# Kernel optimization log

Hardware: AMD Instinct MI355X
Metric: run time of the kernel (lower is better)

The kernel has to match this reference:

```python
import jax, jax.numpy as jnp
import numpy as np
from jax.ops import segment_sum

IN_DIM, HID_DIM, OUT_DIM = 128, 128, 64
N_NODES, N_EDGES = 50000, 800000


def gcn_conv(x, src, dst, W, b, n_nodes):
    # Symmetric GCN normalization (no self loops): deg at targets from unit weights
    deg = segment_sum(jnp.ones(src.shape[0], dtype=x.dtype), dst, num_segments=n_nodes)
    dinv = jnp.where(deg > 0, jax.lax.rsqrt(jnp.maximum(deg, 1.0)), 0.0)
    norm = dinv[src] * dinv[dst]                      # [E]
    h = x @ W                                         # [N, out] small GEMM first (PyG order)
    msg = h[src] * norm[:, None]                      # gather + scale: [E, out]
    out = segment_sum(msg, dst, num_segments=n_nodes) # scatter-add to targets
    return out + b


def setup_inputs() -> dict:
    key = jax.random.key(0)
    k1, k2, k3, k4, k5 = jax.random.split(key, 5)
    x = jax.random.normal(k1, (N_NODES, IN_DIM), dtype=jnp.float32)
    edge_index = jax.random.randint(k2, (2, N_EDGES), 0, N_NODES, dtype=jnp.int64)
    s1 = 1.0 / np.sqrt(IN_DIM)
    s2 = 1.0 / np.sqrt(HID_DIM)
    W1 = jax.random.uniform(k3, (IN_DIM, HID_DIM), jnp.float32, -s1, s1)
    b1 = jnp.zeros((HID_DIM,), jnp.float32)
    W2 = jax.random.uniform(k4, (HID_DIM, OUT_DIM), jnp.float32, -s2, s2)
    b2 = jnp.zeros((OUT_DIM,), jnp.float32)
    return {"x": x, "edge_index": edge_index, "W1": W1, "b1": b1, "W2": W2, "b2": b2}


def reference(x, edge_index, W1, b1, W2, b2):
    n_nodes = x.shape[0]
    src, dst = edge_index[0], edge_index[1]
    h = gcn_conv(x, src, dst, W1, b1, n_nodes)
    h = jax.nn.relu(h)
    # Dropout is identity in eval mode (reference is deterministic)
    out = gcn_conv(h, src, dst, W2, b2, n_nodes)
    return out
```

## Files before the change

### kernel.cpp

```cpp
#include <hip/hip_runtime.h>

#define N_NODES 50000
#define N_EDGES 800000
#define IN_DIM  128
#define HID_DIM 128
#define OUT_DIM 64

#define NPAD 50176
#define CAP  64
#define GEMM1B ((N_NODES + 63) / 64)
#define FILLB (N_EDGES / 256)
#define W2PREPB 8

typedef __attribute__((ext_vector_type(8))) short bf16x8;
typedef __attribute__((ext_vector_type(4))) float f32x4;
typedef __attribute__((ext_vector_type(2))) float f32x2;

__device__ __forceinline__ unsigned short f2bf(float f) {
    unsigned u = __float_as_uint(f);
    u += 0x7fffu + ((u >> 16) & 1u);
    return (unsigned short)(u >> 16);
}
__device__ __forceinline__ float bflo(unsigned u) { return __uint_as_float(u << 16); }
__device__ __forceinline__ float bfhi(unsigned u) { return __uint_as_float(u & 0xffff0000u); }

#define ACC8(u)  do { \
    acc[0] += bflo(u.x); acc[1] += bfhi(u.x); \
    acc[2] += bflo(u.y); acc[3] += bfhi(u.y); \
    acc[4] += bflo(u.z); acc[5] += bfhi(u.z); \
    acc[6] += bflo(u.w); acc[7] += bfhi(u.w); } while (0)

__device__ __forceinline__ unsigned char f2fp8(float f) {
    return (unsigned char)(__builtin_amdgcn_cvt_pk_fp8_f32(f, f, 0, false) & 0xff);
}

#define ACCF16(u)  do { \
    f32x2 p0 = __builtin_amdgcn_cvt_pk_f32_fp8((int)u.x, false); \
    f32x2 p1 = __builtin_amdgcn_cvt_pk_f32_fp8((int)u.x, true);  \
    f32x2 p2 = __builtin_amdgcn_cvt_pk_f32_fp8((int)u.y, false); \
    f32x2 p3 = __builtin_amdgcn_cvt_pk_f32_fp8((int)u.y, true);  \
    f32x2 p4 = __builtin_amdgcn_cvt_pk_f32_fp8((int)u.z, false); \
    f32x2 p5 = __builtin_amdgcn_cvt_pk_f32_fp8((int)u.z, true);  \
    f32x2 p6 = __builtin_amdgcn_cvt_pk_f32_fp8((int)u.w, false); \
    f32x2 p7 = __builtin_amdgcn_cvt_pk_f32_fp8((int)u.w, true);  \
    acc[0]  += p0[0]; acc[1]  += p0[1]; acc[2]  += p1[0]; acc[3]  += p1[1]; \
    acc[4]  += p2[0]; acc[5]  += p2[1]; acc[6]  += p3[0]; acc[7]  += p3[1]; \
    acc[8]  += p4[0]; acc[9]  += p4[1]; acc[10] += p5[0]; acc[11] += p5[1]; \
    acc[12] += p6[0]; acc[13] += p6[1]; acc[14] += p7[0]; acc[15] += p7[1]; } while (0)

__device__ __forceinline__ float deg2dinv(int deg) {
    return (deg > 0) ? rsqrtf((float)deg) : 0.0f;
}

#define W1T_STRIDE 136


__global__ __launch_bounds__(256) void prep_fill_kernel(const int* __restrict__ src,
                                                        const int* __restrict__ dst,
                                                        int* __restrict__ cnt,
                                                        unsigned short* __restrict__ csr_src,
                                                        const float* __restrict__ W2,
                                                        unsigned short* __restrict__ w2t) {
    int bid = blockIdx.x;
    int tid = threadIdx.x;
    if (bid < W2PREPB) {
        int idx = bid * 256 + tid;
        int c = idx >> 5, k4 = (idx & 31) * 4;
        ushort4 o;
        o.x = f2bf(W2[(k4 + 0) * 64 + c]);
        o.y = f2bf(W2[(k4 + 1) * 64 + c]);
        o.z = f2bf(W2[(k4 + 2) * 64 + c]);
        o.w = f2bf(W2[(k4 + 3) * 64 + c]);
        *(ushort4*)(w2t + c * 128 + k4) = o;
    } else {
        int e = (bid - W2PREPB) * 256 + tid;
        int s = src[e], d = dst[e];
        int slot = atomicAdd(&cnt[d], 1);
        if (slot < CAP) csr_src[(d << 6) + slot] = (unsigned short)s;
    }
}


__global__ __launch_bounds__(256) void gemm1_kernel(const float* __restrict__ x,
                                                    const float* __restrict__ W1,
                                                    const int* __restrict__ cnt,
                                                    unsigned char* __restrict__ h1f8) {
    __shared__ unsigned short w1t[128 * W1T_STRIDE];

    int tid = threadIdx.x;
#pragma unroll
    for (int i = 0; i < 64; ++i) {
        int idx = i * 256 + tid;
        int k = idx >> 7, c = idx & 127;
        w1t[c * W1T_STRIDE + k] = f2bf(W1[idx]);
    }
    __syncthreads();

    int wave = tid >> 6;
    int lane = tid & 63;
    int n = lane & 15, quad = lane >> 4;
    int row0 = blockIdx.x * 64 + wave * 16;

    int arow = row0 + n;
    if (arow >= N_NODES) arow = N_NODES - 1;
    const float* aptr = x + (size_t)arow * 128 + quad * 8;
    const unsigned short* bbase = w1t + (size_t)n * W1T_STRIDE + quad * 8;

    f32x4 acc[8];
#pragma unroll
    for (int t = 0; t < 8; ++t) acc[t] = (f32x4){0.f, 0.f, 0.f, 0.f};

#pragma unroll
    for (int w4 = 0; w4 < 4; ++w4) {
        float4 f0 = *(const float4*)(aptr + w4 * 32);
        float4 f1 = *(const float4*)(aptr + w4 * 32 + 4);
        bf16x8 af;
        af[0] = (short)f2bf(f0.x); af[1] = (short)f2bf(f0.y);
        af[2] = (short)f2bf(f0.z); af[3] = (short)f2bf(f0.w);
        af[4] = (short)f2bf(f1.x); af[5] = (short)f2bf(f1.y);
        af[6] = (short)f2bf(f1.z); af[7] = (short)f2bf(f1.w);
#pragma unroll
        for (int t = 0; t < 8; ++t) {
            bf16x8 bf = *(const bf16x8*)(bbase + (size_t)t * 16 * W1T_STRIDE + w4 * 32);
            acc[t] = __builtin_amdgcn_mfma_f32_16x16x32_bf16(af, bf, acc[t], 0, 0, 0);
        }
    }

#pragma unroll
    for (int r = 0; r < 4; ++r) {
        int row = row0 + quad * 4 + r;
        if (row < N_NODES) {
            float dn = deg2dinv(cnt[row]);
            unsigned char* o = h1f8 + (size_t)row * 128 + n;
#pragma unroll
            for (int t = 0; t < 8; ++t) o[t * 16] = f2fp8(acc[t][r] * dn);
        }
    }
}


#define A1T_STRIDE 136

__global__ __launch_bounds__(1024) void agg1_gemm2_fused(const unsigned short* __restrict__ csr_src,
                                                         const int* __restrict__ cnt,
                                                         const float* __restrict__ b1,
                                                         const unsigned char* __restrict__ h1f8,
                                                         const unsigned short* __restrict__ w2t,
                                                         unsigned short* __restrict__ h2b) {
    __shared__ unsigned short a1t[16 * A1T_STRIDE];

    int node0 = blockIdx.x * 16;
    int wave = threadIdx.x >> 6;
    int lane = threadIdx.x & 63;
    int grp = lane >> 3;
    int q   = lane & 7;
    int node = node0 + wave;
    int start = node << 6;
    int m = cnt[node];
    float dn = deg2dinv(m);
    if (m > CAP) m = CAP;

    float acc[16] = {};
    int j = grp;
    for (; j + 8 < m; j += 16) {
        int s0 = csr_src[start + j];
        int s1 = csr_src[start + j + 8];
        uint4 u0 = ((const uint4*)(h1f8 + (size_t)s0 * 128))[q];
        uint4 u1 = ((const uint4*)(h1f8 + (size_t)s1 * 128))[q];
        ACCF16(u0); ACCF16(u1);
    }
    if (j < m) {
        int s0 = csr_src[start + j];
        uint4 u0 = ((const uint4*)(h1f8 + (size_t)s0 * 128))[q];
        ACCF16(u0);
    }

#pragma unroll
    for (int d = 8; d <= 32; d <<= 1) {
#pragma unroll
        for (int c = 0; c < 16; ++c) acc[c] += __shfl_xor(acc[c], d, 64);
    }

    if (grp == 0) {
        int c0 = q * 16;
        float4 bA = *(const float4*)(b1 + c0);
        float4 bB = *(const float4*)(b1 + c0 + 4);
        float4 bC = *(const float4*)(b1 + c0 + 8);
        float4 bD = *(const float4*)(b1 + c0 + 12);
        ushort4 oA, oB, oC, oD;
        oA.x = f2bf(fmaxf(acc[0]  * dn + bA.x, 0.f));
        oA.y = f2bf(fmaxf(acc[1]  * dn + bA.y, 0.f));
        oA.z = f2bf(fmaxf(acc[2]  * dn + bA.z, 0.f));
        oA.w = f2bf(fmaxf(acc[3]  * dn + bA.w, 0.f));
        oB.x = f2bf(fmaxf(acc[4]  * dn + bB.x, 0.f));
        oB.y = f2bf(fmaxf(acc[5]  * dn + bB.y, 0.f));
        oB.z = f2bf(fmaxf(acc[6]  * dn + bB.z, 0.f));
        oB.w = f2bf(fmaxf(acc[7]  * dn + bB.w, 0.f));
        oC.x = f2bf(fmaxf(acc[8]  * dn + bC.x, 0.f));
        oC.y = f2bf(fmaxf(acc[9]  * dn + bC.y, 0.f));
        oC.z = f2bf(fmaxf(acc[10] * dn + bC.z, 0.f));
        oC.w = f2bf(fmaxf(acc[11] * dn + bC.w, 0.f));
        oD.x = f2bf(fmaxf(acc[12] * dn + bD.x, 0.f));
        oD.y = f2bf(fmaxf(acc[13] * dn + bD.y, 0.f));
        oD.z = f2bf(fmaxf(acc[14] * dn + bD.z, 0.f));
        oD.w = f2bf(fmaxf(acc[15] * dn + bD.w, 0.f));
        ushort4* o = (ushort4*)(a1t + wave * A1T_STRIDE + c0);
        o[0] = oA; o[1] = oB; o[2] = oC; o[3] = oD;
    }
    __syncthreads();

    if (wave < 4) {
        int n = lane & 15, quad = lane >> 4;
        const unsigned short* bbase = w2t + (size_t)(wave * 16 + n) * 128 + quad * 8;
        const unsigned short* abase = a1t + (size_t)n * A1T_STRIDE + quad * 8;

        f32x4 c2 = (f32x4){0.f, 0.f, 0.f, 0.f};
#pragma unroll
        for (int w4 = 0; w4 < 4; ++w4) {
            bf16x8 af = *(const bf16x8*)(abase + w4 * 32);
            bf16x8 bf = *(const bf16x8*)(bbase + w4 * 32);
            c2 = __builtin_amdgcn_mfma_f32_16x16x32_bf16(af, bf, c2, 0, 0, 0);
        }

#pragma unroll
        for (int r = 0; r < 4; ++r) {
            int row = node0 + quad * 4 + r;
            float dr = deg2dinv(cnt[row]);
            h2b[(size_t)row * 64 + wave * 16 + n] = f2bf(c2[r] * dr);
        }
    }
}


__global__ __launch_bounds__(256) void agg2_kernel(const unsigned short* __restrict__ csr_src,
                                                   const int* __restrict__ cnt,
                                                   const float* __restrict__ b2,
                                                   const unsigned short* __restrict__ h2b,
                                                   float* __restrict__ out) {
    int node = blockIdx.x * 4 + (threadIdx.x >> 6);
    if (node >= N_NODES) return;
    int lane = threadIdx.x & 63;
    int grp = lane >> 3;
    int q   = lane & 7;
    int start = node << 6;
    int m = cnt[node];
    float dn = deg2dinv(m);
    if (m > CAP) m = CAP;

    float acc[8] = {};

    int j = grp;
    for (; j + 8 < m; j += 16) {
        int s0 = csr_src[start + j];
        int s1 = csr_src[start + j + 8];
        uint4 u0 = ((const uint4*)(h2b + (size_t)s0 * 64))[q];
        uint4 u1 = ((const uint4*)(h2b + (size_t)s1 * 64))[q];
        ACC8(u0); ACC8(u1);
    }
    if (j < m) {
        int s0 = csr_src[start + j];
        uint4 u0 = ((const uint4*)(h2b + (size_t)s0 * 64))[q];
        ACC8(u0);
    }

#pragma unroll
    for (int d = 8; d <= 32; d <<= 1) {
#pragma unroll
        for (int c = 0; c < 8; ++c) acc[c] += __shfl_xor(acc[c], d, 64);
    }

    if (lane < 8) {
        float4 bA = ((const float4*)b2)[2 * q];
        float4 bB = ((const float4*)b2)[2 * q + 1];
        float4 rA, rB;
        rA.x = acc[0] * dn + bA.x;
        rA.y = acc[1] * dn + bA.y;
        rA.z = acc[2] * dn + bA.z;
        rA.w = acc[3] * dn + bA.w;
        rB.x = acc[4] * dn + bB.x;
        rB.y = acc[5] * dn + bB.y;
        rB.z = acc[6] * dn + bB.z;
        rB.w = acc[7] * dn + bB.w;
        float4* o = (float4*)(out + (size_t)node * 64);
        o[2 * q] = rA;
        o[2 * q + 1] = rB;
    }
}


extern "C" void kernel_launch(void* const* d_in, const int* in_sizes, int n_in,
                              void* d_out, int out_size, void* d_ws, size_t ws_size,
                              hipStream_t stream) {
    const float* x  = (const float*)d_in[0];
    const int*   ei = (const int*)d_in[1];
    const float* W1 = (const float*)d_in[2];
    const float* b1 = (const float*)d_in[3];
    const float* W2 = (const float*)d_in[4];
    const float* b2 = (const float*)d_in[5];
    float* out = (float*)d_out;

    const int* src = ei;
    const int* dst = ei + N_EDGES;

    char* ws = (char*)d_ws;
    int*   cnt       = (int*)ws;
    unsigned short* csr_src = (unsigned short*)(cnt + NPAD);
    unsigned char* h1f8 = (unsigned char*)(csr_src + (size_t)N_NODES * CAP);
    unsigned short* h2b = (unsigned short*)(h1f8 + (size_t)N_NODES * HID_DIM);
    unsigned short* w2t = h2b + (size_t)N_NODES * OUT_DIM;

    (void)hipMemsetAsync(cnt, 0, NPAD * sizeof(int), stream);

    prep_fill_kernel<<<W2PREPB + FILLB, 256, 0, stream>>>(src, dst, cnt, csr_src,
                                                          W2, w2t);

    gemm1_kernel<<<GEMM1B, 256, 0, stream>>>(x, W1, cnt, h1f8);

    agg1_gemm2_fused<<<N_NODES / 16, 1024, 0, stream>>>(csr_src, cnt, b1, h1f8, w2t, h2b);

    agg2_kernel<<<(N_NODES + 3) / 4, 256, 0, stream>>>(csr_src, cnt, b2, h2b, out);
}
```

Baseline: 199.3 us.

## Remap agg1 to 8 lanes per node, dropping cross-lane shuffle reductions

The fused layer-1 aggregation plus GEMM2 kernel now gives each node an 8-lane group instead of a full 64-lane wave, so 32 nodes share a 256-thread block. Each group walks all of its node's edges serially, loading four source indices at once as a ushort4. This removes the three-step shuffle-xor reduction across 16 accumulators and the idle lanes on low-degree nodes. All four waves now run two 16-row MFMA tiles for GEMM2 instead of leaving waves idle. In exchange each lane carries a longer dependent gather chain with less memory-level parallelism per node, and bounds checks are added for the last partial block.

```diff
diff --git a/kernel.cpp b/kernel.cpp
--- a/kernel.cpp
+++ b/kernel.cpp
@@ -11,6 +11,7 @@
 #define GEMM1B ((N_NODES + 63) / 64)
 #define FILLB (N_EDGES / 256)
 #define W2PREPB 8
+#define AGG1B ((N_NODES + 31) / 32)
 
 typedef __attribute__((ext_vector_type(8))) short bf16x8;
 typedef __attribute__((ext_vector_type(4))) float f32x4;
@@ -141,47 +142,44 @@
 
 #define A1T_STRIDE 136
 
-__global__ __launch_bounds__(1024) void agg1_gemm2_fused(const unsigned short* __restrict__ csr_src,
-                                                         const int* __restrict__ cnt,
-                                                         const float* __restrict__ b1,
-                                                         const unsigned char* __restrict__ h1f8,
-                                                         const unsigned short* __restrict__ w2t,
-                                                         unsigned short* __restrict__ h2b) {
-    __shared__ unsigned short a1t[16 * A1T_STRIDE];
-
-    int node0 = blockIdx.x * 16;
-    int wave = threadIdx.x >> 6;
-    int lane = threadIdx.x & 63;
-    int grp = lane >> 3;
-    int q   = lane & 7;
-    int node = node0 + wave;
+__global__ __launch_bounds__(256) void agg1_gemm2_fused(const unsigned short* __restrict__ csr_src,
+                                                        const int* __restrict__ cnt,
+                                                        const float* __restrict__ b1,
+                                                        const unsigned char* __restrict__ h1f8,
+                                                        const unsigned short* __restrict__ w2t,
+                                                        unsigned short* __restrict__ h2b) {
+    __shared__ unsigned short a1t[32 * A1T_STRIDE];
+
+    int node0 = blockIdx.x * 32;
+    int g = threadIdx.x >> 3;
+    int q = threadIdx.x & 7;
+    int node = node0 + g;
+    int m = 0;
+    float dn = 0.f;
+    if (node < N_NODES) {
+        m = cnt[node];
+        dn = deg2dinv(m);
+        if (m > CAP) m = CAP;
+    }
     int start = node << 6;
-    int m = cnt[node];
-    float dn = deg2dinv(m);
-    if (m > CAP) m = CAP;
 
     float acc[16] = {};
-    int j = grp;
-    for (; j + 8 < m; j += 16) {
-        int s0 = csr_src[start + j];
-        int s1 = csr_src[start + j + 8];
-        uint4 u0 = ((const uint4*)(h1f8 + (size_t)s0 * 128))[q];
-        uint4 u1 = ((const uint4*)(h1f8 + (size_t)s1 * 128))[q];
-        ACCF16(u0); ACCF16(u1);
-    }
-    if (j < m) {
+    int j = 0;
+    for (; j + 3 < m; j += 4) {
+        ushort4 sa = *(const ushort4*)(csr_src + start + j);
+        uint4 u0 = ((const uint4*)(h1f8 + (size_t)sa.x * 128))[q];
+        uint4 u1 = ((const uint4*)(h1f8 + (size_t)sa.y * 128))[q];
+        uint4 u2 = ((const uint4*)(h1f8 + (size_t)sa.z * 128))[q];
+        uint4 u3 = ((const uint4*)(h1f8 + (size_t)sa.w * 128))[q];
+        ACCF16(u0); ACCF16(u1); ACCF16(u2); ACCF16(u3);
+    }
+    for (; j < m; ++j) {
         int s0 = csr_src[start + j];
         uint4 u0 = ((const uint4*)(h1f8 + (size_t)s0 * 128))[q];
         ACCF16(u0);
     }
 
-#pragma unroll
-    for (int d = 8; d <= 32; d <<= 1) {
-#pragma unroll
-        for (int c = 0; c < 16; ++c) acc[c] += __shfl_xor(acc[c], d, 64);
-    }
-
-    if (grp == 0) {
+    {
         int c0 = q * 16;
         float4 bA = *(const float4*)(b1 + c0);
         float4 bB = *(const float4*)(b1 + c0 + 4);
@@ -204,16 +202,19 @@
         oD.y = f2bf(fmaxf(acc[13] * dn + bD.y, 0.f));
         oD.z = f2bf(fmaxf(acc[14] * dn + bD.z, 0.f));
         oD.w = f2bf(fmaxf(acc[15] * dn + bD.w, 0.f));
-        ushort4* o = (ushort4*)(a1t + wave * A1T_STRIDE + c0);
+        ushort4* o = (ushort4*)(a1t + g * A1T_STRIDE + c0);
         o[0] = oA; o[1] = oB; o[2] = oC; o[3] = oD;
     }
     __syncthreads();
 
-    if (wave < 4) {
-        int n = lane & 15, quad = lane >> 4;
-        const unsigned short* bbase = w2t + (size_t)(wave * 16 + n) * 128 + quad * 8;
-        const unsigned short* abase = a1t + (size_t)n * A1T_STRIDE + quad * 8;
-
+    int wave = threadIdx.x >> 6;
+    int lane = threadIdx.x & 63;
+    int n = lane & 15, quad = lane >> 4;
+    const unsigned short* bbase = w2t + (size_t)(wave * 16 + n) * 128 + quad * 8;
+
+#pragma unroll
+    for (int rb = 0; rb < 2; ++rb) {
+        const unsigned short* abase = a1t + (size_t)(rb * 16 + n) * A1T_STRIDE + quad * 8;
         f32x4 c2 = (f32x4){0.f, 0.f, 0.f, 0.f};
 #pragma unroll
         for (int w4 = 0; w4 < 4; ++w4) {
@@ -221,12 +222,13 @@
             bf16x8 bf = *(const bf16x8*)(bbase + w4 * 32);
             c2 = __builtin_amdgcn_mfma_f32_16x16x32_bf16(af, bf, c2, 0, 0, 0);
         }
-
 #pragma unroll
         for (int r = 0; r < 4; ++r) {
-            int row = node0 + quad * 4 + r;
-            float dr = deg2dinv(cnt[row]);
-            h2b[(size_t)row * 64 + wave * 16 + n] = f2bf(c2[r] * dr);
+            int row = node0 + rb * 16 + quad * 4 + r;
+            if (row < N_NODES) {
+                float dr = deg2dinv(cnt[row]);
+                h2b[(size_t)row * 64 + wave * 16 + n] = f2bf(c2[r] * dr);
+            }
         }
     }
 }
@@ -316,7 +318,7 @@
 
     gemm1_kernel<<<GEMM1B, 256, 0, stream>>>(x, W1, cnt, h1f8);
 
-    agg1_gemm2_fused<<<N_NODES / 16, 1024, 0, stream>>>(csr_src, cnt, b1, h1f8, w2t, h2b);
+    agg1_gemm2_fused<<<AGG1B, 256, 0, stream>>>(csr_src, cnt, b1, h1f8, w2t, h2b);
 
     agg2_kernel<<<(N_NODES + 3) / 4, 256, 0, stream>>>(csr_src, cnt, b2, h2b, out);
 }
```

New measurement: 187.6 us. -5.9%, faster.
